# Optimization experiments

Hardware: AMD Instinct MI355X
Metric: run time of the kernel (lower is better)

## Reference

```python
import jax, jax.numpy as jnp
import numpy as np

N_NODES = 100000
N_EDGES = 3200000
BN_EPS = 1e-5


def setup_inputs() -> dict:
    key = jax.random.key(0)
    ks = jax.random.split(key, 16)
    return {
        "x": jax.random.normal(ks[0], (N_NODES, 2), jnp.float32),
        "eq_labels": jax.random.randint(ks[1], (N_NODES,), 0, 32, jnp.int32),
        "edge_index": jax.random.randint(ks[2], (2, N_EDGES), 0, N_NODES, jnp.int32),
        "eq_emb": jax.random.normal(ks[3], (32, 8), jnp.float32),
        "W1_0": jax.random.normal(ks[4], (10, 64), jnp.float32) * 0.3,
        "b1_0": jnp.zeros((64,), jnp.float32),
        "W2_0": jax.random.normal(ks[5], (64, 64), jnp.float32) * 0.12,
        "b2_0": jnp.zeros((64,), jnp.float32),
        "eps_0": jnp.zeros((), jnp.float32),
        "gamma_0": jnp.ones((64,), jnp.float32),
        "beta_0": jnp.zeros((64,), jnp.float32),
        "W1_s": jax.random.normal(ks[6], (2, 64, 64), jnp.float32) * 0.12,
        "b1_s": jnp.zeros((2, 64), jnp.float32),
        "W2_s": jax.random.normal(ks[7], (2, 64, 64), jnp.float32) * 0.12,
        "b2_s": jnp.zeros((2, 64), jnp.float32),
        "eps_s": jnp.zeros((2,), jnp.float32),
        "gamma_s": jnp.ones((2, 64), jnp.float32),
        "beta_s": jnp.zeros((2, 64), jnp.float32),
        "Wf": jax.random.normal(ks[8], (64, 1), jnp.float32) * 0.12,
        "bf": jnp.zeros((1,), jnp.float32),
    }


def _gin_bn_relu(h, src, dst, W1, b1, W2, b2, eps, gamma, beta):
    # GINConv: (1+eps)*x_i + sum_{j->i} x_j, then 2-layer ReLU MLP, then BN, ReLU
    agg = jax.ops.segment_sum(h[src], dst, num_segments=N_NODES)
    h = (1.0 + eps) * h + agg
    h = jax.nn.relu(h @ W1 + b1)
    h = jax.nn.relu(h @ W2 + b2)
    mu = jnp.mean(h, axis=0)
    var = jnp.var(h, axis=0)
    h = (h - mu) * jax.lax.rsqrt(var + BN_EPS) * gamma + beta
    return jax.nn.relu(h)


def reference(x, eq_labels, edge_index, eq_emb, W1_0, b1_0, W2_0, b2_0, eps_0,
              gamma_0, beta_0, W1_s, b1_s, W2_s, b2_s, eps_s, gamma_s, beta_s,
              Wf, bf):
    src, dst = edge_index[0], edge_index[1]
    h = jnp.concatenate([x, eq_emb[eq_labels]], axis=-1)  # [N, 10]
    h = _gin_bn_relu(h, src, dst, W1_0, b1_0, W2_0, b2_0, eps_0, gamma_0, beta_0)
    for i in range(2):
        h = _gin_bn_relu(h, src, dst, W1_s[i], b1_s[i], W2_s[i], b2_s[i],
                         eps_s[i], gamma_s[i], beta_s[i])
    return (h @ Wf + bf).squeeze(-1)  # [N]
```

## Files before the change

kernel.cpp:

```cpp
#include <hip/hip_runtime.h>

#define N_NODES 100000
#define N_EDGES 3200000
#define BN_EPS 1e-5f

#define BLK_NODES 128
#define NBLK 782
#define CHUNK 16384
#define NW ((N_EDGES + CHUNK - 1) / CHUNK)
#define BCAP 4480
#define CUR_PAD 16
#define NSLICE 32

typedef unsigned int uint;
typedef unsigned short ushort;

__device__ inline float bf_lo(uint u) { return __uint_as_float(u << 16); }
__device__ inline float bf_hi(uint u) { return __uint_as_float(u & 0xffff0000u); }
__device__ inline ushort f2bf(float a) {
    uint ua = __float_as_uint(a); ua += 0x7fffu + ((ua >> 16) & 1u);
    return (ushort)(ua >> 16);
}

__global__ __launch_bounds__(256) void k_h0(const float* __restrict__ x,
                                            const int* __restrict__ lab,
                                            const float* __restrict__ emb,
                                            float* __restrict__ h0, int n) {
    int i = blockIdx.x * blockDim.x + threadIdx.x;
    if (i >= n) return;
    float v[16];
    v[0] = x[2 * i];
    v[1] = x[2 * i + 1];
    int L = lab[i];
#pragma unroll
    for (int k = 0; k < 8; k++) v[2 + k] = emb[L * 8 + k];
#pragma unroll
    for (int k = 10; k < 16; k++) v[k] = 0.f;
    float4* o = (float4*)(h0 + (size_t)i * 16);
#pragma unroll
    for (int q = 0; q < 4; q++) {
        float4 t;
        t.x = v[4 * q]; t.y = v[4 * q + 1]; t.z = v[4 * q + 2]; t.w = v[4 * q + 3];
        o[q] = t;
    }
}

__global__ __launch_bounds__(256) void k_fill(const int* __restrict__ src,
                                              const int* __restrict__ dst,
                                              int* __restrict__ gcur,
                                              int* __restrict__ bucket) {
    __shared__ int cnt[NBLK];
    __shared__ int off[NBLK];
    int t = threadIdx.x;
    for (int b = t; b < NBLK; b += 256) cnt[b] = 0;
    __syncthreads();
    int my0 = blockIdx.x * CHUNK + t * 64;
    for (int k = 0; k < 64; k += 4) {
        int e = my0 + k;
        if (e + 3 < N_EDGES) {
            int4 d4 = *(const int4*)(dst + e);
            atomicAdd(&cnt[d4.x >> 7], 1);
            atomicAdd(&cnt[d4.y >> 7], 1);
            atomicAdd(&cnt[d4.z >> 7], 1);
            atomicAdd(&cnt[d4.w >> 7], 1);
        } else {
#pragma unroll
            for (int kk = 0; kk < 4; kk++) {
                int ee = e + kk;
                if (ee < N_EDGES) atomicAdd(&cnt[dst[ee] >> 7], 1);
            }
        }
    }
    __syncthreads();
    for (int b = t; b < NBLK; b += 256) {
        int c = cnt[b];
        off[b] = (c > 0) ? atomicAdd(&gcur[b * CUR_PAD], c) : 0;
    }
    __syncthreads();
    for (int k = 0; k < 64; k += 4) {
        int e = my0 + k;
        if (e + 3 < N_EDGES) {
            int4 d4 = *(const int4*)(dst + e);
            int4 s4 = *(const int4*)(src + e);
            int dd[4] = {d4.x, d4.y, d4.z, d4.w};
            int ss[4] = {s4.x, s4.y, s4.z, s4.w};
#pragma unroll
            for (int kk = 0; kk < 4; kk++) {
                int b = dd[kk] >> 7;
                int p = atomicAdd(&off[b], 1);
                if (p < BCAP)
                    bucket[(size_t)b * BCAP + p] = ((dd[kk] & 127) << 17) | ss[kk];
            }
        } else {
#pragma unroll
            for (int kk = 0; kk < 4; kk++) {
                int ee = e + kk;
                if (ee < N_EDGES) {
                    int d = dst[ee], s = src[ee];
                    int b = d >> 7;
                    int p = atomicAdd(&off[b], 1);
                    if (p < BCAP)
                        bucket[(size_t)b * BCAP + p] = ((d & 127) << 17) | s;
                }
            }
        }
    }
}

__global__ __launch_bounds__(256) void k_sort(const int* __restrict__ gcur,
                                              const int* __restrict__ bucket,
                                              int* __restrict__ col2,
                                              int2* __restrict__ nodeoff, int n) {
    __shared__ int cnt[BLK_NODES];
    __shared__ int scn[BLK_NODES];
    __shared__ int cur[BLK_NODES];
    int t = threadIdx.x;
    int blk = blockIdx.x;
    if (t < BLK_NODES) cnt[t] = 0;
    __syncthreads();
    int cc = min(gcur[blk * CUR_PAD], BCAP);
    const int* bb = bucket + (size_t)blk * BCAP;
    for (int i = t; i < cc; i += 256) atomicAdd(&cnt[bb[i] >> 17], 1);
    __syncthreads();
    if (t < BLK_NODES) scn[t] = cnt[t];
    __syncthreads();
#pragma unroll
    for (int off = 1; off < BLK_NODES; off <<= 1) {
        int v = (t >= off && t < BLK_NODES) ? scn[t - off] : 0;
        __syncthreads();
        if (t < BLK_NODES) scn[t] += v;
        __syncthreads();
    }
    if (t < BLK_NODES) {
        int start = scn[t] - cnt[t];
        cur[t] = start;
        int node = blk * BLK_NODES + t;
        if (node < n) nodeoff[node] = int2{blk * BCAP + start, cnt[t]};
    }
    __syncthreads();
    int* out = col2 + (size_t)blk * BCAP;
    for (int i = t; i < cc; i += 256) {
        int w = bb[i];
        int p = atomicAdd(&cur[w >> 17], 1);
        out[p] = w & 0x1FFFF;
    }
}

__global__ __launch_bounds__(256) void k_layer0(const float* __restrict__ h0,
                                                const int* __restrict__ nodeoff,
                                                const int* __restrict__ col,
                                                const float* __restrict__ epsp,
                                                const float* __restrict__ W1,
                                                const float* __restrict__ b1,
                                                const float* __restrict__ W2,
                                                const float* __restrict__ b2,
                                                float* __restrict__ hraw,
                                                float* __restrict__ part_out) {
    __shared__ float xb[4][2][16];
    __shared__ float yb[4][2][64];
    __shared__ float sb[4][128];
    int t = threadIdx.x;
    int w = t >> 6;
    int lane = t & 63;
    int pairId = blockIdx.x * 4 + w;
    int hl = lane >> 5, l5 = lane & 31;
    int node = pairId * 2 + hl;
    int q = l5 & 3, g = l5 >> 2;
    const float4* h4 = (const float4*)h0;
    int4 no = *(const int4*)(nodeoff + pairId * 4);
    int start = hl ? no.z : no.x;
    int deg = hl ? no.w : no.y;
    int mx = max(no.y, no.w);
    const int* cl = col + start;
    float ep = 1.f + *epsp;
    float ac[4] = {0.f, 0.f, 0.f, 0.f};

    int wv = (deg > 0) ? cl[min(l5, deg - 1)] : 0;
    int wv2 = 0;
    if (mx > 32) wv2 = (deg > 32) ? cl[min(32 + l5, deg - 1)] : wv;
    int idx[4], idx2[4];
#pragma unroll
    for (int i = 0; i < 4; i++) idx[i] = __shfl(wv, (hl << 5) + g + 8 * i, 64);
    float4 rows[4], rows2[4];
#pragma unroll
    for (int i = 0; i < 4; i++) rows[i] = h4[(size_t)idx[i] * 4 + q];
    if (mx > 32) {
#pragma unroll
        for (int i = 0; i < 4; i++) idx2[i] = __shfl(wv2, (hl << 5) + g + 8 * i, 64);
#pragma unroll
        for (int i = 0; i < 4; i++) rows2[i] = h4[(size_t)idx2[i] * 4 + q];
    }
#pragma unroll
    for (int i = 0; i < 4; i++) {
        float m = (g + 8 * i < deg) ? 1.f : 0.f;
        ac[0] = fmaf(m, rows[i].x, ac[0]);
        ac[1] = fmaf(m, rows[i].y, ac[1]);
        ac[2] = fmaf(m, rows[i].z, ac[2]);
        ac[3] = fmaf(m, rows[i].w, ac[3]);
    }
    if (mx > 32) {
#pragma unroll
        for (int i = 0; i < 4; i++) {
            float m = (32 + g + 8 * i < deg) ? 1.f : 0.f;
            ac[0] = fmaf(m, rows2[i].x, ac[0]);
            ac[1] = fmaf(m, rows2[i].y, ac[1]);
            ac[2] = fmaf(m, rows2[i].z, ac[2]);
            ac[3] = fmaf(m, rows2[i].w, ac[3]);
        }
        for (int e = 64 + g; e < deg; e += 8) {
            float4 v = h4[(size_t)cl[e] * 4 + q];
            ac[0] += v.x; ac[1] += v.y; ac[2] += v.z; ac[3] += v.w;
        }
    }
#pragma unroll
    for (int off2 = 4; off2 < 32; off2 <<= 1) {
#pragma unroll
        for (int k = 0; k < 4; k++) ac[k] += __shfl_xor(ac[k], off2, 64);
    }
    {
        float4 xi = h4[(size_t)node * 4 + q];
        ac[0] = fmaf(ep, xi.x, ac[0]);
        ac[1] = fmaf(ep, xi.y, ac[1]);
        ac[2] = fmaf(ep, xi.z, ac[2]);
        ac[3] = fmaf(ep, xi.w, ac[3]);
    }
    if (g == 0) *(float4*)&xb[w][hl][q * 4] = float4{ac[0], ac[1], ac[2], ac[3]};
    float4 a0 = *(float4*)&xb[w][0][0];
    float4 a1 = *(float4*)&xb[w][0][4];
    float2 a2 = *(float2*)&xb[w][0][8];
    float4 c0 = *(float4*)&xb[w][1][0];
    float4 c1 = *(float4*)&xb[w][1][4];
    float2 c2 = *(float2*)&xb[w][1][8];
    float h1A = b1[lane], h1B = h1A;
    float wg;
    wg = W1[0 * 64 + lane]; h1A = fmaf(a0.x, wg, h1A); h1B = fmaf(c0.x, wg, h1B);
    wg = W1[1 * 64 + lane]; h1A = fmaf(a0.y, wg, h1A); h1B = fmaf(c0.y, wg, h1B);
    wg = W1[2 * 64 + lane]; h1A = fmaf(a0.z, wg, h1A); h1B = fmaf(c0.z, wg, h1B);
    wg = W1[3 * 64 + lane]; h1A = fmaf(a0.w, wg, h1A); h1B = fmaf(c0.w, wg, h1B);
    wg = W1[4 * 64 + lane]; h1A = fmaf(a1.x, wg, h1A); h1B = fmaf(c1.x, wg, h1B);
    wg = W1[5 * 64 + lane]; h1A = fmaf(a1.y, wg, h1A); h1B = fmaf(c1.y, wg, h1B);
    wg = W1[6 * 64 + lane]; h1A = fmaf(a1.z, wg, h1A); h1B = fmaf(c1.z, wg, h1B);
    wg = W1[7 * 64 + lane]; h1A = fmaf(a1.w, wg, h1A); h1B = fmaf(c1.w, wg, h1B);
    wg = W1[8 * 64 + lane]; h1A = fmaf(a2.x, wg, h1A); h1B = fmaf(c2.x, wg, h1B);
    wg = W1[9 * 64 + lane]; h1A = fmaf(a2.y, wg, h1A); h1B = fmaf(c2.y, wg, h1B);
    h1A = fmaxf(h1A, 0.f);
    h1B = fmaxf(h1B, 0.f);
    yb[w][0][lane] = h1A;
    yb[w][1][lane] = h1B;
    float h2A = b2[lane], h2B = h2A;
#pragma unroll
    for (int k0 = 0; k0 < 64; k0 += 4) {
        float4 ya = *(float4*)&yb[w][0][k0];
        float4 yc = *(float4*)&yb[w][1][k0];
        wg = W2[(k0 + 0) * 64 + lane]; h2A = fmaf(ya.x, wg, h2A); h2B = fmaf(yc.x, wg, h2B);
        wg = W2[(k0 + 1) * 64 + lane]; h2A = fmaf(ya.y, wg, h2A); h2B = fmaf(yc.y, wg, h2B);
        wg = W2[(k0 + 2) * 64 + lane]; h2A = fmaf(ya.z, wg, h2A); h2B = fmaf(yc.z, wg, h2B);
        wg = W2[(k0 + 3) * 64 + lane]; h2A = fmaf(ya.w, wg, h2A); h2B = fmaf(yc.w, wg, h2B);
    }
    float rA = fmaxf(h2A, 0.f), rB = fmaxf(h2B, 0.f);
    sb[w][lane] = rA + rB;
    sb[w][64 + lane] = rA * rA + rB * rB;
    __syncthreads();
    if (t < 128) {
        float tot = sb[0][t] + sb[1][t] + sb[2][t] + sb[3][t];
        atomicAdd(&part_out[(blockIdx.x & (NSLICE - 1)) * 128 + t], tot);
    }
    hraw[(size_t)(pairId * 2 + 0) * 64 + lane] = rA;
    hraw[(size_t)(pairId * 2 + 1) * 64 + lane] = rB;
}

__global__ __launch_bounds__(256) void k_act(const float* __restrict__ hraw,
                                             const float* __restrict__ part,
                                             const float* __restrict__ gamma,
                                             const float* __restrict__ beta,
                                             ushort* __restrict__ act, float invn) {
    __shared__ float st[128];
    __shared__ float sc[64], sh[64];
    int t = threadIdx.x;
    if (t < 128) {
        float S = 0.f;
#pragma unroll 8
        for (int s = 0; s < NSLICE; s++) S += part[s * 128 + t];
        st[t] = S;
    }
    __syncthreads();
    if (t < 64) {
        float mu = st[t] * invn;
        float var = fmaxf(st[64 + t] * invn - mu * mu, 0.f);
        float s = gamma[t] * rsqrtf(var + BN_EPS);
        sc[t] = s;
        sh[t] = beta[t] - mu * s;
    }
    __syncthreads();
    int base = (blockIdx.x * 256 + t) * 4;
    int f0 = base & 63;
    float4 v = *(const float4*)(hraw + base);
    float a0 = fmaxf(fmaf(v.x, sc[f0 + 0], sh[f0 + 0]), 0.f);
    float a1 = fmaxf(fmaf(v.y, sc[f0 + 1], sh[f0 + 1]), 0.f);
    float a2 = fmaxf(fmaf(v.z, sc[f0 + 2], sh[f0 + 2]), 0.f);
    float a3 = fmaxf(fmaf(v.w, sc[f0 + 3], sh[f0 + 3]), 0.f);
    uint2 o;
    o.x = (uint)f2bf(a0) | ((uint)f2bf(a1) << 16);
    o.y = (uint)f2bf(a2) | ((uint)f2bf(a3) << 16);
    *(uint2*)(act + base) = o;
}

__global__ __launch_bounds__(256) void k_layer(const uint* __restrict__ actin,
                                               const int* __restrict__ nodeoff,
                                               const int* __restrict__ col,
                                               const float* __restrict__ epsp,
                                               const float* __restrict__ W1,
                                               const float* __restrict__ b1,
                                               const float* __restrict__ W2,
                                               const float* __restrict__ b2,
                                               float* __restrict__ hraw,
                                               float* __restrict__ part_out) {
    __shared__ float xb[4][2][64];
    __shared__ float yb[4][2][64];
    __shared__ float sb[4][128];
    int t = threadIdx.x;
    int w = t >> 6;
    int lane = t & 63;
    int pairId = blockIdx.x * 4 + w;
    int hl = lane >> 5, l5 = lane & 31;
    int node = pairId * 2 + hl;
    int q = l5 & 7, g = l5 >> 3;
    const uint4* hb4 = (const uint4*)actin;
    int4 no = *(const int4*)(nodeoff + pairId * 4);
    int start = hl ? no.z : no.x;
    int deg = hl ? no.w : no.y;
    int mx = max(no.y, no.w);
    const int* cl = col + start;
    float ep = 1.f + *epsp;
    float acc[8];
#pragma unroll
    for (int k = 0; k < 8; k++) acc[k] = 0.f;

    auto procm = [&](uint4 v, float m) {
        acc[0] = fmaf(m, bf_lo(v.x), acc[0]);
        acc[1] = fmaf(m, bf_hi(v.x), acc[1]);
        acc[2] = fmaf(m, bf_lo(v.y), acc[2]);
        acc[3] = fmaf(m, bf_hi(v.y), acc[3]);
        acc[4] = fmaf(m, bf_lo(v.z), acc[4]);
        acc[5] = fmaf(m, bf_hi(v.z), acc[5]);
        acc[6] = fmaf(m, bf_lo(v.w), acc[6]);
        acc[7] = fmaf(m, bf_hi(v.w), acc[7]);
    };

    int wv = (deg > 0) ? cl[min(l5, deg - 1)] : 0;
    int wv2 = 0;
    if (mx > 32) wv2 = (deg > 32) ? cl[min(32 + l5, deg - 1)] : wv;
    int idx[4], idx2[4];
#pragma unroll
    for (int i = 0; i < 4; i++) idx[i] = __shfl(wv, (hl << 5) + g + 4 * i, 64);
    uint4 rows[4], rows2[4];
#pragma unroll
    for (int i = 0; i < 4; i++) rows[i] = hb4[(size_t)idx[i] * 8 + q];
    if (mx > 32) {
#pragma unroll
        for (int i = 0; i < 4; i++) idx2[i] = __shfl(wv2, (hl << 5) + g + 4 * i, 64);
#pragma unroll
        for (int i = 0; i < 4; i++) rows2[i] = hb4[(size_t)idx2[i] * 8 + q];
    }
#pragma unroll
    for (int i = 0; i < 4; i++) procm(rows[i], (g + 4 * i < deg) ? 1.f : 0.f);
    if (mx > 32) {
#pragma unroll
        for (int i = 0; i < 4; i++) procm(rows2[i], (32 + g + 4 * i < deg) ? 1.f : 0.f);
        for (int e = 64 + g; e < deg; e += 4) procm(hb4[(size_t)cl[e] * 8 + q], 1.f);
    }
#pragma unroll
    for (int i = 0; i < 4; i++) {
        int src2 = (hl << 5) + g + 4 * (i + 4);
        int id = __shfl(wv, src2, 64);
        if (g + 4 * (i + 4) < 32) {
            uint4 v = hb4[(size_t)id * 8 + q];
            procm(v, (g + 4 * (i + 4) < deg) ? 1.f : 0.f);
        }
    }
    if (mx > 32) {
#pragma unroll
        for (int i = 0; i < 4; i++) {
            int src2 = (hl << 5) + g + 4 * (i + 4);
            int id = __shfl(wv2, src2, 64);
            uint4 v = hb4[(size_t)id * 8 + q];
            procm(v, (32 + g + 4 * (i + 4) < deg) ? 1.f : 0.f);
        }
    }
#pragma unroll
    for (int off2 = 8; off2 < 32; off2 <<= 1) {
#pragma unroll
        for (int k = 0; k < 8; k++) acc[k] += __shfl_xor(acc[k], off2, 64);
    }
    {
        uint4 v = hb4[(size_t)node * 8 + q];
        acc[0] = fmaf(ep, bf_lo(v.x), acc[0]);
        acc[1] = fmaf(ep, bf_hi(v.x), acc[1]);
        acc[2] = fmaf(ep, bf_lo(v.y), acc[2]);
        acc[3] = fmaf(ep, bf_hi(v.y), acc[3]);
        acc[4] = fmaf(ep, bf_lo(v.z), acc[4]);
        acc[5] = fmaf(ep, bf_hi(v.z), acc[5]);
        acc[6] = fmaf(ep, bf_lo(v.w), acc[6]);
        acc[7] = fmaf(ep, bf_hi(v.w), acc[7]);
    }
    if (g == 0) {
        *(float4*)&xb[w][hl][q * 8 + 0] = float4{acc[0], acc[1], acc[2], acc[3]};
        *(float4*)&xb[w][hl][q * 8 + 4] = float4{acc[4], acc[5], acc[6], acc[7]};
    }
    float h1A = b1[lane], h1B = h1A;
    float wg;
#pragma unroll
    for (int f0 = 0; f0 < 64; f0 += 4) {
        float4 xa = *(float4*)&xb[w][0][f0];
        float4 xc = *(float4*)&xb[w][1][f0];
        wg = W1[(f0 + 0) * 64 + lane]; h1A = fmaf(xa.x, wg, h1A); h1B = fmaf(xc.x, wg, h1B);
        wg = W1[(f0 + 1) * 64 + lane]; h1A = fmaf(xa.y, wg, h1A); h1B = fmaf(xc.y, wg, h1B);
        wg = W1[(f0 + 2) * 64 + lane]; h1A = fmaf(xa.z, wg, h1A); h1B = fmaf(xc.z, wg, h1B);
        wg = W1[(f0 + 3) * 64 + lane]; h1A = fmaf(xa.w, wg, h1A); h1B = fmaf(xc.w, wg, h1B);
    }
    h1A = fmaxf(h1A, 0.f);
    h1B = fmaxf(h1B, 0.f);
    yb[w][0][lane] = h1A;
    yb[w][1][lane] = h1B;
    float h2A = b2[lane], h2B = h2A;
#pragma unroll
    for (int k0 = 0; k0 < 64; k0 += 4) {
        float4 ya = *(float4*)&yb[w][0][k0];
        float4 yc = *(float4*)&yb[w][1][k0];
        wg = W2[(k0 + 0) * 64 + lane]; h2A = fmaf(ya.x, wg, h2A); h2B = fmaf(yc.x, wg, h2B);
        wg = W2[(k0 + 1) * 64 + lane]; h2A = fmaf(ya.y, wg, h2A); h2B = fmaf(yc.y, wg, h2B);
        wg = W2[(k0 + 2) * 64 + lane]; h2A = fmaf(ya.z, wg, h2A); h2B = fmaf(yc.z, wg, h2B);
        wg = W2[(k0 + 3) * 64 + lane]; h2A = fmaf(ya.w, wg, h2A); h2B = fmaf(yc.w, wg, h2B);
    }
    float rA = fmaxf(h2A, 0.f), rB = fmaxf(h2B, 0.f);
    sb[w][lane] = rA + rB;
    sb[w][64 + lane] = rA * rA + rB * rB;
    __syncthreads();
    if (t < 128) {
        float tot = sb[0][t] + sb[1][t] + sb[2][t] + sb[3][t];
        atomicAdd(&part_out[(blockIdx.x & (NSLICE - 1)) * 128 + t], tot);
    }
    hraw[(size_t)(pairId * 2 + 0) * 64 + lane] = rA;
    hraw[(size_t)(pairId * 2 + 1) * 64 + lane] = rB;
}

__global__ __launch_bounds__(256) void k_out(const float* __restrict__ hraw,
                                             const float* __restrict__ part,
                                             const float* __restrict__ gamma,
                                             const float* __restrict__ beta,
                                             const float* __restrict__ Wf,
                                             const float* __restrict__ bfp,
                                             float* __restrict__ out, int n,
                                             float invn) {
    __shared__ float st[128];
    __shared__ float sc[64], sh[64];
    int t = threadIdx.x;
    if (t < 128) {
        float S = 0.f;
#pragma unroll 8
        for (int s = 0; s < NSLICE; s++) S += part[s * 128 + t];
        st[t] = S;
    }
    __syncthreads();
    if (t < 64) {
        float mu = st[t] * invn;
        float var = fmaxf(st[64 + t] * invn - mu * mu, 0.f);
        float s = gamma[t] * rsqrtf(var + BN_EPS);
        sc[t] = s;
        sh[t] = beta[t] - mu * s;
    }
    __syncthreads();
    int i = blockIdx.x * blockDim.x + threadIdx.x;
    if (i >= n) return;
    float acc = *bfp;
    const float4* h4 = (const float4*)(hraw + (size_t)i * 64);
#pragma unroll
    for (int qq = 0; qq < 16; qq++) {
        float4 v = h4[qq];
        int j = qq * 4;
        acc = fmaf(fmaxf(fmaf(v.x, sc[j + 0], sh[j + 0]), 0.f), Wf[j + 0], acc);
        acc = fmaf(fmaxf(fmaf(v.y, sc[j + 1], sh[j + 1]), 0.f), Wf[j + 1], acc);
        acc = fmaf(fmaxf(fmaf(v.z, sc[j + 2], sh[j + 2]), 0.f), Wf[j + 2], acc);
        acc = fmaf(fmaxf(fmaf(v.w, sc[j + 3], sh[j + 3]), 0.f), Wf[j + 3], acc);
    }
    out[i] = acc;
}

extern "C" void kernel_launch(void* const* d_in, const int* in_sizes, int n_in,
                              void* d_out, int out_size, void* d_ws, size_t ws_size,
                              hipStream_t stream) {
    const float* x      = (const float*)d_in[0];
    const int*   lab    = (const int*)d_in[1];
    const int*   edge   = (const int*)d_in[2];
    const float* emb    = (const float*)d_in[3];
    const float* W1_0   = (const float*)d_in[4];
    const float* b1_0   = (const float*)d_in[5];
    const float* W2_0   = (const float*)d_in[6];
    const float* b2_0   = (const float*)d_in[7];
    const float* eps_0  = (const float*)d_in[8];
    const float* gamma_0= (const float*)d_in[9];
    const float* beta_0 = (const float*)d_in[10];
    const float* W1_s   = (const float*)d_in[11];
    const float* b1_s   = (const float*)d_in[12];
    const float* W2_s   = (const float*)d_in[13];
    const float* b2_s   = (const float*)d_in[14];
    const float* eps_s  = (const float*)d_in[15];
    const float* gamma_s= (const float*)d_in[16];
    const float* beta_s = (const float*)d_in[17];
    const float* Wf     = (const float*)d_in[18];
    const float* bf     = (const float*)d_in[19];

    const int N = N_NODES, E = N_EDGES;
    const int* srcp = edge;
    const int* dstp = edge + E;

    char* p = (char*)d_ws;
    auto alloc = [&](size_t bytes) {
        void* r = (void*)p;
        p += (bytes + 255) & ~(size_t)255;
        return r;
    };
    int* bucket  = (int*)alloc((size_t)NBLK * BCAP * 4);
    int* col2    = (int*)alloc((size_t)NBLK * BCAP * 4);
    int* gcur    = (int*)alloc((size_t)NBLK * CUR_PAD * 4);
    int* nodeoff = (int*)alloc((size_t)N * 8);
    float* hraw  = (float*)alloc((size_t)N * 64 * 4);
    ushort* act  = (ushort*)alloc((size_t)N * 64 * 2);
    float* h0    = (float*)alloc((size_t)N * 16 * 4);
    float* parts = (float*)alloc(3 * NSLICE * 128 * 4);

    hipMemsetAsync(gcur, 0, (size_t)NBLK * CUR_PAD * 4, stream);
    hipMemsetAsync(parts, 0, 3 * NSLICE * 128 * 4, stream);

    const int TB = 256;
    const int gN = (N + TB - 1) / TB;
    const int gL = N / 8;
    const int gA = N * 64 / 1024;
    const float invn = 1.0f / (float)N;

    k_h0<<<gN, TB, 0, stream>>>(x, lab, emb, h0, N);
    k_fill<<<NW, TB, 0, stream>>>(srcp, dstp, gcur, bucket);
    k_sort<<<NBLK, TB, 0, stream>>>(gcur, bucket, col2, (int2*)nodeoff, N);

    k_layer0<<<gL, TB, 0, stream>>>(h0, nodeoff, col2, eps_0,
                                    W1_0, b1_0, W2_0, b2_0, hraw,
                                    parts + 0 * NSLICE * 128);
    k_act<<<gA, TB, 0, stream>>>(hraw, parts + 0 * NSLICE * 128, gamma_0, beta_0,
                                 act, invn);

    k_layer<<<gL, TB, 0, stream>>>((const uint*)act, nodeoff, col2, eps_s + 0,
                                   W1_s + 0 * 4096, b1_s + 0 * 64,
                                   W2_s + 0 * 4096, b2_s + 0 * 64, hraw,
                                   parts + 1 * NSLICE * 128);
    k_act<<<gA, TB, 0, stream>>>(hraw, parts + 1 * NSLICE * 128, gamma_s + 0 * 64,
                                 beta_s + 0 * 64, act, invn);

    k_layer<<<gL, TB, 0, stream>>>((const uint*)act, nodeoff, col2, eps_s + 1,
                                   W1_s + 1 * 4096, b1_s + 1 * 64,
                                   W2_s + 1 * 4096, b2_s + 1 * 64, hraw,
                                   parts + 2 * NSLICE * 128);

    k_out<<<gN, TB, 0, stream>>>(hraw, parts + 2 * NSLICE * 128,
                                 gamma_s + 1 * 64, beta_s + 1 * 64, Wf, bf,
                                 (float*)d_out, N, invn);
}
```

Before: 444.0 us.

## Use fp16 MFMA for per-node GIN MLPs over 16-node wave tiles

```diff
diff --git a/kernel.cpp b/kernel.cpp
--- a/kernel.cpp
+++ b/kernel.cpp
@@ -14,12 +14,39 @@
 
 typedef unsigned int uint;
 typedef unsigned short ushort;
+typedef _Float16 half_t;
+typedef __attribute__((ext_vector_type(8))) _Float16 h8v;
+typedef __attribute__((ext_vector_type(4))) float f4v;
 
 __device__ inline float bf_lo(uint u) { return __uint_as_float(u << 16); }
 __device__ inline float bf_hi(uint u) { return __uint_as_float(u & 0xffff0000u); }
 __device__ inline ushort f2bf(float a) {
     uint ua = __float_as_uint(a); ua += 0x7fffu + ((ua >> 16) & 1u);
     return (ushort)(ua >> 16);
+}
+__device__ inline ushort f2h(float a) {
+    union { half_t h; ushort u; } r;
+    r.h = (half_t)a;
+    return r.u;
+}
+__device__ inline h8v packAh(const float* v) {
+    h8v r;
+#pragma unroll
+    for (int i = 0; i < 8; i++) r[i] = (half_t)v[i];
+    return r;
+}
+__device__ inline h8v loadH(const ushort* p) {
+    union { uint4 q; h8v f; } r;
+    r.q = *(const uint4*)p;
+    return r.f;
+}
+__device__ inline h8v loadHh(const half_t* p) {
+    union { uint4 q; h8v f; } r;
+    r.q = *(const uint4*)p;
+    return r.f;
+}
+__device__ inline f4v mfma16(h8v a, h8v b, f4v c) {
+    return __builtin_amdgcn_mfma_f32_16x16x32_f16(a, b, c, 0, 0, 0);
 }
 
 __global__ __launch_bounds__(256) void k_h0(const float* __restrict__ x,
@@ -45,6 +72,33 @@
     }
 }
 
+__global__ __launch_bounds__(256) void k_wcvt(const float* __restrict__ W1_0,
+                                              const float* __restrict__ W2_0,
+                                              const float* __restrict__ W1_s,
+                                              const float* __restrict__ W2_s,
+                                              ushort* __restrict__ W0t,
+                                              ushort* __restrict__ W20t,
+                                              ushort* __restrict__ Wst) {
+    int t = threadIdx.x;
+    for (int i = t; i < 64 * 32; i += 256) {
+        int n = i >> 5, k = i & 31;
+        W0t[i] = (k < 10) ? f2h(W1_0[k * 64 + n]) : (ushort)0;
+    }
+    for (int i = t; i < 4096; i += 256) {
+        int n = i >> 6, k = i & 63;
+        W20t[i] = f2h(W2_0[k * 64 + n]);
+    }
+    for (int l = 0; l < 2; l++) {
+        const float* w1 = W1_s + l * 4096;
+        const float* w2 = W2_s + l * 4096;
+        for (int i = t; i < 4096; i += 256) {
+            int n = i >> 6, k = i & 63;
+            Wst[l * 8192 + i] = f2h(w1[k * 64 + n]);
+            Wst[l * 8192 + 4096 + i] = f2h(w2[k * 64 + n]);
+        }
+    }
+}
+
 __global__ __launch_bounds__(256) void k_fill(const int* __restrict__ src,
                                               const int* __restrict__ dst,
                                               int* __restrict__ gcur,
@@ -146,127 +200,151 @@
     }
 }
 
-__global__ __launch_bounds__(256) void k_layer0(const float* __restrict__ h0,
-                                                const int* __restrict__ nodeoff,
-                                                const int* __restrict__ col,
-                                                const float* __restrict__ epsp,
-                                                const float* __restrict__ W1,
-                                                const float* __restrict__ b1,
-                                                const float* __restrict__ W2,
-                                                const float* __restrict__ b2,
-                                                float* __restrict__ hraw,
-                                                float* __restrict__ part_out) {
-    __shared__ float xb[4][2][16];
-    __shared__ float yb[4][2][64];
-    __shared__ float sb[4][128];
-    int t = threadIdx.x;
-    int w = t >> 6;
-    int lane = t & 63;
-    int pairId = blockIdx.x * 4 + w;
+__global__ __launch_bounds__(256) void k_layer0M(const float* __restrict__ h0,
+                                                 const int* __restrict__ nodeoff,
+                                                 const int* __restrict__ col,
+                                                 const float* __restrict__ epsp,
+                                                 const ushort* __restrict__ W0t,
+                                                 const float* __restrict__ b1,
+                                                 const ushort* __restrict__ W20t,
+                                                 const float* __restrict__ b2,
+                                                 float* __restrict__ hraw,
+                                                 float* __restrict__ part_out) {
+    __shared__ float comb[4][16][36];
+    __shared__ half_t h1s[4][16][72];
+    int t = threadIdx.x, w = t >> 6, lane = t & 63;
+    int base = blockIdx.x * 64 + w * 16;
+    float ep = 1.f + *epsp;
     int hl = lane >> 5, l5 = lane & 31;
-    int node = pairId * 2 + hl;
     int q = l5 & 3, g = l5 >> 2;
     const float4* h4 = (const float4*)h0;
-    int4 no = *(const int4*)(nodeoff + pairId * 4);
-    int start = hl ? no.z : no.x;
-    int deg = hl ? no.w : no.y;
-    int mx = max(no.y, no.w);
-    const int* cl = col + start;
-    float ep = 1.f + *epsp;
-    float ac[4] = {0.f, 0.f, 0.f, 0.f};
-
-    int wv = (deg > 0) ? cl[min(l5, deg - 1)] : 0;
-    int wv2 = 0;
-    if (mx > 32) wv2 = (deg > 32) ? cl[min(32 + l5, deg - 1)] : wv;
-    int idx[4], idx2[4];
-#pragma unroll
-    for (int i = 0; i < 4; i++) idx[i] = __shfl(wv, (hl << 5) + g + 8 * i, 64);
-    float4 rows[4], rows2[4];
-#pragma unroll
-    for (int i = 0; i < 4; i++) rows[i] = h4[(size_t)idx[i] * 4 + q];
-    if (mx > 32) {
-#pragma unroll
-        for (int i = 0; i < 4; i++) idx2[i] = __shfl(wv2, (hl << 5) + g + 8 * i, 64);
-#pragma unroll
-        for (int i = 0; i < 4; i++) rows2[i] = h4[(size_t)idx2[i] * 4 + q];
-    }
-#pragma unroll
-    for (int i = 0; i < 4; i++) {
-        float m = (g + 8 * i < deg) ? 1.f : 0.f;
-        ac[0] = fmaf(m, rows[i].x, ac[0]);
-        ac[1] = fmaf(m, rows[i].y, ac[1]);
-        ac[2] = fmaf(m, rows[i].z, ac[2]);
-        ac[3] = fmaf(m, rows[i].w, ac[3]);
-    }
-    if (mx > 32) {
-#pragma unroll
-        for (int i = 0; i < 4; i++) {
-            float m = (32 + g + 8 * i < deg) ? 1.f : 0.f;
-            ac[0] = fmaf(m, rows2[i].x, ac[0]);
-            ac[1] = fmaf(m, rows2[i].y, ac[1]);
-            ac[2] = fmaf(m, rows2[i].z, ac[2]);
-            ac[3] = fmaf(m, rows2[i].w, ac[3]);
-        }
-        for (int e = 64 + g; e < deg; e += 8) {
-            float4 v = h4[(size_t)cl[e] * 4 + q];
-            ac[0] += v.x; ac[1] += v.y; ac[2] += v.z; ac[3] += v.w;
-        }
-    }
-#pragma unroll
-    for (int off2 = 4; off2 < 32; off2 <<= 1) {
-#pragma unroll
-        for (int k = 0; k < 4; k++) ac[k] += __shfl_xor(ac[k], off2, 64);
-    }
+
+#pragma unroll 2
+    for (int r = 0; r < 8; r++) {
+        int nodeA = base + 2 * r, nodeB = nodeA + 1;
+        int4 no = *(const int4*)(nodeoff + nodeA * 2);
+        int degA = (nodeA < N_NODES) ? no.y : 0;
+        int degB = (nodeB < N_NODES) ? no.w : 0;
+        int start = hl ? no.z : no.x;
+        int deg = hl ? degB : degA;
+        int mx = max(degA, degB);
+        const int* cl = col + start;
+        float ac[4] = {0.f, 0.f, 0.f, 0.f};
+        if (mx > 0) {
+            int wv = (deg > 0) ? cl[min(l5, deg - 1)] : 0;
+            int idx[4];
+#pragma unroll
+            for (int i = 0; i < 4; i++) idx[i] = __shfl(wv, (hl << 5) + g + 8 * i, 64);
+            float4 rows[4];
+#pragma unroll
+            for (int i = 0; i < 4; i++) rows[i] = h4[(size_t)idx[i] * 4 + q];
+#pragma unroll
+            for (int i = 0; i < 4; i++) {
+                float m = (g + 8 * i < deg) ? 1.f : 0.f;
+                ac[0] = fmaf(m, rows[i].x, ac[0]);
+                ac[1] = fmaf(m, rows[i].y, ac[1]);
+                ac[2] = fmaf(m, rows[i].z, ac[2]);
+                ac[3] = fmaf(m, rows[i].w, ac[3]);
+            }
+            if (mx > 32) {
+                int wv2 = (deg > 32) ? cl[min(32 + l5, deg - 1)] : wv;
+                int idx2[4];
+#pragma unroll
+                for (int i = 0; i < 4; i++) idx2[i] = __shfl(wv2, (hl << 5) + g + 8 * i, 64);
+                float4 rows2[4];
+#pragma unroll
+                for (int i = 0; i < 4; i++) rows2[i] = h4[(size_t)idx2[i] * 4 + q];
+#pragma unroll
+                for (int i = 0; i < 4; i++) {
+                    float m = (32 + g + 8 * i < deg) ? 1.f : 0.f;
+                    ac[0] = fmaf(m, rows2[i].x, ac[0]);
+                    ac[1] = fmaf(m, rows2[i].y, ac[1]);
+                    ac[2] = fmaf(m, rows2[i].z, ac[2]);
+                    ac[3] = fmaf(m, rows2[i].w, ac[3]);
+                }
+                for (int e = 64 + g; e < deg; e += 8) {
+                    float4 v = h4[(size_t)cl[e] * 4 + q];
+                    ac[0] += v.x; ac[1] += v.y; ac[2] += v.z; ac[3] += v.w;
+                }
+            }
+        }
+#pragma unroll
+        for (int o = 4; o < 32; o <<= 1) {
+#pragma unroll
+            for (int k = 0; k < 4; k++) ac[k] += __shfl_xor(ac[k], o, 64);
+        }
+        int node = hl ? nodeB : nodeA;
+        bool valid = node < N_NODES;
+        int nodeC = valid ? node : 0;
+        float vm = valid ? ep : 0.f;
+        float4 xi = h4[(size_t)nodeC * 4 + q];
+        ac[0] = fmaf(vm, xi.x, ac[0]);
+        ac[1] = fmaf(vm, xi.y, ac[1]);
+        ac[2] = fmaf(vm, xi.z, ac[2]);
+        ac[3] = fmaf(vm, xi.w, ac[3]);
+        if (!valid) { ac[0] = ac[1] = ac[2] = ac[3] = 0.f; }
+        if (g == 0) {
+            int nl = 2 * r + hl;
+            *(float4*)&comb[w][nl][q * 4] = float4{ac[0], ac[1], ac[2], ac[3]};
+            *(float4*)&comb[w][nl][16 + q * 4] = float4{0.f, 0.f, 0.f, 0.f};
+        }
+    }
+    int mr = lane & 15, kq = lane >> 4, nc = lane & 15;
+    h8v A0;
     {
-        float4 xi = h4[(size_t)node * 4 + q];
-        ac[0] = fmaf(ep, xi.x, ac[0]);
-        ac[1] = fmaf(ep, xi.y, ac[1]);
-        ac[2] = fmaf(ep, xi.z, ac[2]);
-        ac[3] = fmaf(ep, xi.w, ac[3]);
-    }
-    if (g == 0) *(float4*)&xb[w][hl][q * 4] = float4{ac[0], ac[1], ac[2], ac[3]};
-    float4 a0 = *(float4*)&xb[w][0][0];
-    float4 a1 = *(float4*)&xb[w][0][4];
-    float2 a2 = *(float2*)&xb[w][0][8];
-    float4 c0 = *(float4*)&xb[w][1][0];
-    float4 c1 = *(float4*)&xb[w][1][4];
-    float2 c2 = *(float2*)&xb[w][1][8];
-    float h1A = b1[lane], h1B = h1A;
-    float wg;
-    wg = W1[0 * 64 + lane]; h1A = fmaf(a0.x, wg, h1A); h1B = fmaf(c0.x, wg, h1B);
-    wg = W1[1 * 64 + lane]; h1A = fmaf(a0.y, wg, h1A); h1B = fmaf(c0.y, wg, h1B);
-    wg = W1[2 * 64 + lane]; h1A = fmaf(a0.z, wg, h1A); h1B = fmaf(c0.z, wg, h1B);
-    wg = W1[3 * 64 + lane]; h1A = fmaf(a0.w, wg, h1A); h1B = fmaf(c0.w, wg, h1B);
-    wg = W1[4 * 64 + lane]; h1A = fmaf(a1.x, wg, h1A); h1B = fmaf(c1.x, wg, h1B);
-    wg = W1[5 * 64 + lane]; h1A = fmaf(a1.y, wg, h1A); h1B = fmaf(c1.y, wg, h1B);
-    wg = W1[6 * 64 + lane]; h1A = fmaf(a1.z, wg, h1A); h1B = fmaf(c1.z, wg, h1B);
-    wg = W1[7 * 64 + lane]; h1A = fmaf(a1.w, wg, h1A); h1B = fmaf(c1.w, wg, h1B);
-    wg = W1[8 * 64 + lane]; h1A = fmaf(a2.x, wg, h1A); h1B = fmaf(c2.x, wg, h1B);
-    wg = W1[9 * 64 + lane]; h1A = fmaf(a2.y, wg, h1A); h1B = fmaf(c2.y, wg, h1B);
-    h1A = fmaxf(h1A, 0.f);
-    h1B = fmaxf(h1B, 0.f);
-    yb[w][0][lane] = h1A;
-    yb[w][1][lane] = h1B;
-    float h2A = b2[lane], h2B = h2A;
-#pragma unroll
-    for (int k0 = 0; k0 < 64; k0 += 4) {
-        float4 ya = *(float4*)&yb[w][0][k0];
-        float4 yc = *(float4*)&yb[w][1][k0];
-        wg = W2[(k0 + 0) * 64 + lane]; h2A = fmaf(ya.x, wg, h2A); h2B = fmaf(yc.x, wg, h2B);
-        wg = W2[(k0 + 1) * 64 + lane]; h2A = fmaf(ya.y, wg, h2A); h2B = fmaf(yc.y, wg, h2B);
-        wg = W2[(k0 + 2) * 64 + lane]; h2A = fmaf(ya.z, wg, h2A); h2B = fmaf(yc.z, wg, h2B);
-        wg = W2[(k0 + 3) * 64 + lane]; h2A = fmaf(ya.w, wg, h2A); h2B = fmaf(yc.w, wg, h2B);
-    }
-    float rA = fmaxf(h2A, 0.f), rB = fmaxf(h2B, 0.f);
-    sb[w][lane] = rA + rB;
-    sb[w][64 + lane] = rA * rA + rB * rB;
-    __syncthreads();
-    if (t < 128) {
-        float tot = sb[0][t] + sb[1][t] + sb[2][t] + sb[3][t];
-        atomicAdd(&part_out[(blockIdx.x & (NSLICE - 1)) * 128 + t], tot);
-    }
-    hraw[(size_t)(pairId * 2 + 0) * 64 + lane] = rA;
-    hraw[(size_t)(pairId * 2 + 1) * 64 + lane] = rB;
+        float a[8];
+        const float* cr = &comb[w][mr][0];
+        *(float4*)&a[0] = *(const float4*)&cr[kq * 8];
+        *(float4*)&a[4] = *(const float4*)&cr[kq * 8 + 4];
+        A0 = packAh(a);
+    }
+#pragma unroll
+    for (int nt = 0; nt < 4; nt++) {
+        float bb = b1[nt * 16 + nc];
+        f4v c = {bb, bb, bb, bb};
+        c = mfma16(A0, loadH(W0t + (nt * 16 + nc) * 32 + kq * 8), c);
+#pragma unroll
+        for (int r2 = 0; r2 < 4; r2++)
+            h1s[w][kq * 4 + r2][nt * 16 + nc] = (half_t)fmaxf(c[r2], 0.f);
+    }
+    h8v P0 = loadHh(&h1s[w][mr][kq * 8]);
+    h8v P1 = loadHh(&h1s[w][mr][32 + kq * 8]);
+    float sA[4], sB[4];
+#pragma unroll
+    for (int nt = 0; nt < 4; nt++) { sA[nt] = 0.f; sB[nt] = 0.f; }
+#pragma unroll
+    for (int nt = 0; nt < 4; nt++) {
+        float bb = b2[nt * 16 + nc];
+        f4v c = {bb, bb, bb, bb};
+        c = mfma16(P0, loadH(W20t + (nt * 16 + nc) * 64 + kq * 8), c);
+        c = mfma16(P1, loadH(W20t + (nt * 16 + nc) * 64 + 32 + kq * 8), c);
+#pragma unroll
+        for (int r2 = 0; r2 < 4; r2++) {
+            int node = base + kq * 4 + r2;
+            float vv = fmaxf(c[r2], 0.f);
+            if (node < N_NODES) {
+                sA[nt] += vv;
+                sB[nt] = fmaf(vv, vv, sB[nt]);
+                hraw[(size_t)node * 64 + nt * 16 + nc] = vv;
+            }
+        }
+    }
+#pragma unroll
+    for (int o = 16; o < 64; o <<= 1) {
+#pragma unroll
+        for (int nt = 0; nt < 4; nt++) {
+            sA[nt] += __shfl_xor(sA[nt], o, 64);
+            sB[nt] += __shfl_xor(sB[nt], o, 64);
+        }
+    }
+    if (kq == 0) {
+        float* pp = part_out + (blockIdx.x & (NSLICE - 1)) * 128;
+#pragma unroll
+        for (int nt = 0; nt < 4; nt++) {
+            atomicAdd(&pp[nt * 16 + nc], sA[nt]);
+            atomicAdd(&pp[64 + nt * 16 + nc], sB[nt]);
+        }
+    }
 }
 
 __global__ __launch_bounds__(256) void k_act(const float* __restrict__ hraw,
@@ -305,143 +383,159 @@
     *(uint2*)(act + base) = o;
 }
 
-__global__ __launch_bounds__(256) void k_layer(const uint* __restrict__ actin,
-                                               const int* __restrict__ nodeoff,
-                                               const int* __restrict__ col,
-                                               const float* __restrict__ epsp,
-                                               const float* __restrict__ W1,
-                                               const float* __restrict__ b1,
-                                               const float* __restrict__ W2,
-                                               const float* __restrict__ b2,
-                                               float* __restrict__ hraw,
-                                               float* __restrict__ part_out) {
-    __shared__ float xb[4][2][64];
-    __shared__ float yb[4][2][64];
-    __shared__ float sb[4][128];
-    int t = threadIdx.x;
-    int w = t >> 6;
-    int lane = t & 63;
-    int pairId = blockIdx.x * 4 + w;
+__global__ __launch_bounds__(256) void k_layerM(const uint* __restrict__ actin,
+                                                const int* __restrict__ nodeoff,
+                                                const int* __restrict__ col,
+                                                const float* __restrict__ epsp,
+                                                const ushort* __restrict__ W1t,
+                                                const float* __restrict__ b1,
+                                                const ushort* __restrict__ W2t,
+                                                const float* __restrict__ b2,
+                                                float* __restrict__ hraw,
+                                                float* __restrict__ part_out) {
+    __shared__ float comb[4][16][68];
+    __shared__ half_t h1s[4][16][72];
+    int t = threadIdx.x, w = t >> 6, lane = t & 63;
+    int base = blockIdx.x * 64 + w * 16;
+    float ep = 1.f + *epsp;
     int hl = lane >> 5, l5 = lane & 31;
-    int node = pairId * 2 + hl;
     int q = l5 & 7, g = l5 >> 3;
     const uint4* hb4 = (const uint4*)actin;
-    int4 no = *(const int4*)(nodeoff + pairId * 4);
-    int start = hl ? no.z : no.x;
-    int deg = hl ? no.w : no.y;
-    int mx = max(no.y, no.w);
-    const int* cl = col + start;
-    float ep = 1.f + *epsp;
-    float acc[8];
-#pragma unroll
-    for (int k = 0; k < 8; k++) acc[k] = 0.f;
-
-    auto procm = [&](uint4 v, float m) {
-        acc[0] = fmaf(m, bf_lo(v.x), acc[0]);
-        acc[1] = fmaf(m, bf_hi(v.x), acc[1]);
-        acc[2] = fmaf(m, bf_lo(v.y), acc[2]);
-        acc[3] = fmaf(m, bf_hi(v.y), acc[3]);
-        acc[4] = fmaf(m, bf_lo(v.z), acc[4]);
-        acc[5] = fmaf(m, bf_hi(v.z), acc[5]);
-        acc[6] = fmaf(m, bf_lo(v.w), acc[6]);
-        acc[7] = fmaf(m, bf_hi(v.w), acc[7]);
-    };
-
-    int wv = (deg > 0) ? cl[min(l5, deg - 1)] : 0;
-    int wv2 = 0;
-    if (mx > 32) wv2 = (deg > 32) ? cl[min(32 + l5, deg - 1)] : wv;
-    int idx[4], idx2[4];
-#pragma unroll
-    for (int i = 0; i < 4; i++) idx[i] = __shfl(wv, (hl << 5) + g + 4 * i, 64);
-    uint4 rows[4], rows2[4];
-#pragma unroll
-    for (int i = 0; i < 4; i++) rows[i] = hb4[(size_t)idx[i] * 8 + q];
-    if (mx > 32) {
-#pragma unroll
-        for (int i = 0; i < 4; i++) idx2[i] = __shfl(wv2, (hl << 5) + g + 4 * i, 64);
-#pragma unroll
-        for (int i = 0; i < 4; i++) rows2[i] = hb4[(size_t)idx2[i] * 8 + q];
-    }
-#pragma unroll
-    for (int i = 0; i < 4; i++) procm(rows[i], (g + 4 * i < deg) ? 1.f : 0.f);
-    if (mx > 32) {
-#pragma unroll
-        for (int i = 0; i < 4; i++) procm(rows2[i], (32 + g + 4 * i < deg) ? 1.f : 0.f);
-        for (int e = 64 + g; e < deg; e += 4) procm(hb4[(size_t)cl[e] * 8 + q], 1.f);
-    }
-#pragma unroll
-    for (int i = 0; i < 4; i++) {
-        int src2 = (hl << 5) + g + 4 * (i + 4);
-        int id = __shfl(wv, src2, 64);
-        if (g + 4 * (i + 4) < 32) {
-            uint4 v = hb4[(size_t)id * 8 + q];
-            procm(v, (g + 4 * (i + 4) < deg) ? 1.f : 0.f);
-        }
-    }
-    if (mx > 32) {
-#pragma unroll
-        for (int i = 0; i < 4; i++) {
-            int src2 = (hl << 5) + g + 4 * (i + 4);
-            int id = __shfl(wv2, src2, 64);
-            uint4 v = hb4[(size_t)id * 8 + q];
-            procm(v, (32 + g + 4 * (i + 4) < deg) ? 1.f : 0.f);
-        }
-    }
-#pragma unroll
-    for (int off2 = 8; off2 < 32; off2 <<= 1) {
-#pragma unroll
-        for (int k = 0; k < 8; k++) acc[k] += __shfl_xor(acc[k], off2, 64);
-    }
+
+#pragma unroll 2
+    for (int r = 0; r < 8; r++) {
+        int nodeA = base + 2 * r, nodeB = nodeA + 1;
+        int4 no = *(const int4*)(nodeoff + nodeA * 2);
+        int degA = (nodeA < N_NODES) ? no.y : 0;
+        int degB = (nodeB < N_NODES) ? no.w : 0;
+        int start = hl ? no.z : no.x;
+        int deg = hl ? degB : degA;
+        int mx = max(degA, degB);
+        const int* cl = col + start;
+        float acc[8];
+#pragma unroll
+        for (int k = 0; k < 8; k++) acc[k] = 0.f;
+        auto procm = [&](uint4 v, float m) {
+            acc[0] = fmaf(m, bf_lo(v.x), acc[0]);
+            acc[1] = fmaf(m, bf_hi(v.x), acc[1]);
+            acc[2] = fmaf(m, bf_lo(v.y), acc[2]);
+            acc[3] = fmaf(m, bf_hi(v.y), acc[3]);
+            acc[4] = fmaf(m, bf_lo(v.z), acc[4]);
+            acc[5] = fmaf(m, bf_hi(v.z), acc[5]);
+            acc[6] = fmaf(m, bf_lo(v.w), acc[6]);
+            acc[7] = fmaf(m, bf_hi(v.w), acc[7]);
+        };
+        if (mx > 0) {
+            int wv = (deg > 0) ? cl[min(l5, deg - 1)] : 0;
+            int idx[8];
+#pragma unroll
+            for (int i = 0; i < 8; i++) idx[i] = __shfl(wv, (hl << 5) + g + 4 * i, 64);
+            uint4 rows[8];
+#pragma unroll
+            for (int i = 0; i < 8; i++) rows[i] = hb4[(size_t)idx[i] * 8 + q];
+#pragma unroll
+            for (int i = 0; i < 8; i++) procm(rows[i], (g + 4 * i < deg) ? 1.f : 0.f);
+            if (mx > 32) {
+                int wv2 = (deg > 32) ? cl[min(32 + l5, deg - 1)] : wv;
+                int idx2[8];
+#pragma unroll
+                for (int i = 0; i < 8; i++) idx2[i] = __shfl(wv2, (hl << 5) + g + 4 * i, 64);
+                uint4 rows2[8];
+#pragma unroll
+                for (int i = 0; i < 8; i++) rows2[i] = hb4[(size_t)idx2[i] * 8 + q];
+#pragma unroll
+                for (int i = 0; i < 8; i++) procm(rows2[i], (32 + g + 4 * i < deg) ? 1.f : 0.f);
+                for (int e = 64 + g; e < deg; e += 4) procm(hb4[(size_t)cl[e] * 8 + q], 1.f);
+            }
+        }
+#pragma unroll
+        for (int o = 8; o < 32; o <<= 1) {
+#pragma unroll
+            for (int k = 0; k < 8; k++) acc[k] += __shfl_xor(acc[k], o, 64);
+        }
+        int node = hl ? nodeB : nodeA;
+        bool valid = node < N_NODES;
+        int nodeC = valid ? node : 0;
+        float vm = valid ? ep : 0.f;
+        uint4 v = hb4[(size_t)nodeC * 8 + q];
+        acc[0] = fmaf(vm, bf_lo(v.x), acc[0]);
+        acc[1] = fmaf(vm, bf_hi(v.x), acc[1]);
+        acc[2] = fmaf(vm, bf_lo(v.y), acc[2]);
+        acc[3] = fmaf(vm, bf_hi(v.y), acc[3]);
+        acc[4] = fmaf(vm, bf_lo(v.z), acc[4]);
+        acc[5] = fmaf(vm, bf_hi(v.z), acc[5]);
+        acc[6] = fmaf(vm, bf_lo(v.w), acc[6]);
+        acc[7] = fmaf(vm, bf_hi(v.w), acc[7]);
+        if (!valid) {
+#pragma unroll
+            for (int k = 0; k < 8; k++) acc[k] = 0.f;
+        }
+        if (g == 0) {
+            int nl = 2 * r + hl;
+            *(float4*)&comb[w][nl][q * 8 + 0] = float4{acc[0], acc[1], acc[2], acc[3]};
+            *(float4*)&comb[w][nl][q * 8 + 4] = float4{acc[4], acc[5], acc[6], acc[7]};
+        }
+    }
+    int mr = lane & 15, kq = lane >> 4, nc = lane & 15;
+    h8v A0, A1;
     {
-        uint4 v = hb4[(size_t)node * 8 + q];
-        acc[0] = fmaf(ep, bf_lo(v.x), acc[0]);
-        acc[1] = fmaf(ep, bf_hi(v.x), acc[1]);
-        acc[2] = fmaf(ep, bf_lo(v.y), acc[2]);
-        acc[3] = fmaf(ep, bf_hi(v.y), acc[3]);
-        acc[4] = fmaf(ep, bf_lo(v.z), acc[4]);
-        acc[5] = fmaf(ep, bf_hi(v.z), acc[5]);
-        acc[6] = fmaf(ep, bf_lo(v.w), acc[6]);
-        acc[7] = fmaf(ep, bf_hi(v.w), acc[7]);
-    }
-    if (g == 0) {
-        *(float4*)&xb[w][hl][q * 8 + 0] = float4{acc[0], acc[1], acc[2], acc[3]};
-        *(float4*)&xb[w][hl][q * 8 + 4] = float4{acc[4], acc[5], acc[6], acc[7]};
-    }
-    float h1A = b1[lane], h1B = h1A;
-    float wg;
-#pragma unroll
-    for (int f0 = 0; f0 < 64; f0 += 4) {
-        float4 xa = *(float4*)&xb[w][0][f0];
-        float4 xc = *(float4*)&xb[w][1][f0];
-        wg = W1[(f0 + 0) * 64 + lane]; h1A = fmaf(xa.x, wg, h1A); h1B = fmaf(xc.x, wg, h1B);
-        wg = W1[(f0 + 1) * 64 + lane]; h1A = fmaf(xa.y, wg, h1A); h1B = fmaf(xc.y, wg, h1B);
-        wg = W1[(f0 + 2) * 64 + lane]; h1A = fmaf(xa.z, wg, h1A); h1B = fmaf(xc.z, wg, h1B);
-        wg = W1[(f0 + 3) * 64 + lane]; h1A = fmaf(xa.w, wg, h1A); h1B = fmaf(xc.w, wg, h1B);
-    }
-    h1A = fmaxf(h1A, 0.f);
-    h1B = fmaxf(h1B, 0.f);
-    yb[w][0][lane] = h1A;
-    yb[w][1][lane] = h1B;
-    float h2A = b2[lane], h2B = h2A;
-#pragma unroll
-    for (int k0 = 0; k0 < 64; k0 += 4) {
-        float4 ya = *(float4*)&yb[w][0][k0];
-        float4 yc = *(float4*)&yb[w][1][k0];
-        wg = W2[(k0 + 0) * 64 + lane]; h2A = fmaf(ya.x, wg, h2A); h2B = fmaf(yc.x, wg, h2B);
-        wg = W2[(k0 + 1) * 64 + lane]; h2A = fmaf(ya.y, wg, h2A); h2B = fmaf(yc.y, wg, h2B);
-        wg = W2[(k0 + 2) * 64 + lane]; h2A = fmaf(ya.z, wg, h2A); h2B = fmaf(yc.z, wg, h2B);
-        wg = W2[(k0 + 3) * 64 + lane]; h2A = fmaf(ya.w, wg, h2A); h2B = fmaf(yc.w, wg, h2B);
-    }
-    float rA = fmaxf(h2A, 0.f), rB = fmaxf(h2B, 0.f);
-    sb[w][lane] = rA + rB;
-    sb[w][64 + lane] = rA * rA + rB * rB;
-    __syncthreads();
-    if (t < 128) {
-        float tot = sb[0][t] + sb[1][t] + sb[2][t] + sb[3][t];
-        atomicAdd(&part_out[(blockIdx.x & (NSLICE - 1)) * 128 + t], tot);
-    }
-    hraw[(size_t)(pairId * 2 + 0) * 64 + lane] = rA;
-    hraw[(size_t)(pairId * 2 + 1) * 64 + lane] = rB;
+        float a[8];
+        const float* cr = &comb[w][mr][0];
+        *(float4*)&a[0] = *(const float4*)&cr[kq * 8];
+        *(float4*)&a[4] = *(const float4*)&cr[kq * 8 + 4];
+        A0 = packAh(a);
+        *(float4*)&a[0] = *(const float4*)&cr[32 + kq * 8];
+        *(float4*)&a[4] = *(const float4*)&cr[32 + kq * 8 + 4];
+        A1 = packAh(a);
+    }
+#pragma unroll
+    for (int nt = 0; nt < 4; nt++) {
+        float bb = b1[nt * 16 + nc];
+        f4v c = {bb, bb, bb, bb};
+        c = mfma16(A0, loadH(W1t + (nt * 16 + nc) * 64 + kq * 8), c);
+        c = mfma16(A1, loadH(W1t + (nt * 16 + nc) * 64 + 32 + kq * 8), c);
+#pragma unroll
+        for (int r2 = 0; r2 < 4; r2++)
+            h1s[w][kq * 4 + r2][nt * 16 + nc] = (half_t)fmaxf(c[r2], 0.f);
+    }
+    h8v P0 = loadHh(&h1s[w][mr][kq * 8]);
+    h8v P1 = loadHh(&h1s[w][mr][32 + kq * 8]);
+    float sA[4], sB[4];
+#pragma unroll
+    for (int nt = 0; nt < 4; nt++) { sA[nt] = 0.f; sB[nt] = 0.f; }
+#pragma unroll
+    for (int nt = 0; nt < 4; nt++) {
+        float bb = b2[nt * 16 + nc];
+        f4v c = {bb, bb, bb, bb};
+        c = mfma16(P0, loadH(W2t + (nt * 16 + nc) * 64 + kq * 8), c);
+        c = mfma16(P1, loadH(W2t + (nt * 16 + nc) * 64 + 32 + kq * 8), c);
+#pragma unroll
+        for (int r2 = 0; r2 < 4; r2++) {
+            int node = base + kq * 4 + r2;
+            float vv = fmaxf(c[r2], 0.f);
+            if (node < N_NODES) {
+                sA[nt] += vv;
+                sB[nt] = fmaf(vv, vv, sB[nt]);
+                hraw[(size_t)node * 64 + nt * 16 + nc] = vv;
+            }
+        }
+    }
+#pragma unroll
+    for (int o = 16; o < 64; o <<= 1) {
+#pragma unroll
+        for (int nt = 0; nt < 4; nt++) {
+            sA[nt] += __shfl_xor(sA[nt], o, 64);
+            sB[nt] += __shfl_xor(sB[nt], o, 64);
+        }
+    }
+    if (kq == 0) {
+        float* pp = part_out + (blockIdx.x & (NSLICE - 1)) * 128;
+#pragma unroll
+        for (int nt = 0; nt < 4; nt++) {
+            atomicAdd(&pp[nt * 16 + nc], sA[nt]);
+            atomicAdd(&pp[64 + nt * 16 + nc], sB[nt]);
+        }
+    }
 }
 
 __global__ __launch_bounds__(256) void k_out(const float* __restrict__ hraw,
@@ -523,42 +617,45 @@
     int* bucket  = (int*)alloc((size_t)NBLK * BCAP * 4);
     int* col2    = (int*)alloc((size_t)NBLK * BCAP * 4);
     int* gcur    = (int*)alloc((size_t)NBLK * CUR_PAD * 4);
-    int* nodeoff = (int*)alloc((size_t)N * 8);
+    int* nodeoff = (int*)alloc((size_t)(N + 64) * 8);
     float* hraw  = (float*)alloc((size_t)N * 64 * 4);
     ushort* act  = (ushort*)alloc((size_t)N * 64 * 2);
     float* h0    = (float*)alloc((size_t)N * 16 * 4);
     float* parts = (float*)alloc(3 * NSLICE * 128 * 4);
+    ushort* W0t  = (ushort*)alloc(64 * 32 * 2);
+    ushort* W20t = (ushort*)alloc(4096 * 2);
+    ushort* Wst  = (ushort*)alloc(2 * 8192 * 2);
 
     hipMemsetAsync(gcur, 0, (size_t)NBLK * CUR_PAD * 4, stream);
     hipMemsetAsync(parts, 0, 3 * NSLICE * 128 * 4, stream);
 
     const int TB = 256;
     const int gN = (N + TB - 1) / TB;
-    const int gL = N / 8;
+    const int gM = (N + 63) / 64;
     const int gA = N * 64 / 1024;
     const float invn = 1.0f / (float)N;
 
     k_h0<<<gN, TB, 0, stream>>>(x, lab, emb, h0, N);
+    k_wcvt<<<1, TB, 0, stream>>>(W1_0, W2_0, W1_s, W2_s, W0t, W20t, Wst);
     k_fill<<<NW, TB, 0, stream>>>(srcp, dstp, gcur, bucket);
     k_sort<<<NBLK, TB, 0, stream>>>(gcur, bucket, col2, (int2*)nodeoff, N);
 
-    k_layer0<<<gL, TB, 0, stream>>>(h0, nodeoff, col2, eps_0,
-                                    W1_0, b1_0, W2_0, b2_0, hraw,
-                                    parts + 0 * NSLICE * 128);
+    k_layer0M<<<gM, TB, 0, stream>>>(h0, nodeoff, col2, eps_0, W0t, b1_0,
+                                     W20t, b2_0, hraw, parts + 0 * NSLICE * 128);
     k_act<<<gA, TB, 0, stream>>>(hraw, parts + 0 * NSLICE * 128, gamma_0, beta_0,
                                  act, invn);
 
-    k_layer<<<gL, TB, 0, stream>>>((const uint*)act, nodeoff, col2, eps_s + 0,
-                                   W1_s + 0 * 4096, b1_s + 0 * 64,
-                                   W2_s + 0 * 4096, b2_s + 0 * 64, hraw,
-                                   parts + 1 * NSLICE * 128);
+    k_layerM<<<gM, TB, 0, stream>>>((const uint*)act, nodeoff, col2, eps_s + 0,
+                                    Wst + 0 * 8192, b1_s + 0 * 64,
+                                    Wst + 0 * 8192 + 4096, b2_s + 0 * 64,
+                                    hraw, parts + 1 * NSLICE * 128);
     k_act<<<gA, TB, 0, stream>>>(hraw, parts + 1 * NSLICE * 128, gamma_s + 0 * 64,
                                  beta_s + 0 * 64, act, invn);
 
-    k_layer<<<gL, TB, 0, stream>>>((const uint*)act, nodeoff, col2, eps_s + 1,
-                                   W1_s + 1 * 4096, b1_s + 1 * 64,
-                                   W2_s + 1 * 4096, b2_s + 1 * 64, hraw,
-                                   parts + 2 * NSLICE * 128);
+    k_layerM<<<gM, TB, 0, stream>>>((const uint*)act, nodeoff, col2, eps_s + 1,
+                                    Wst + 1 * 8192, b1_s + 1 * 64,
+                                    Wst + 1 * 8192 + 4096, b2_s + 1 * 64,
+                                    hraw, parts + 2 * NSLICE * 128);
 
     k_out<<<gN, TB, 0, stream>>>(hraw, parts + 2 * NSLICE * 128,
                                  gamma_s + 1 * 64, beta_s + 1 * 64, Wf, bf,
```

Measured after the change: 433.8 us. 2.3% less time.
